# Optimization experiments

Hardware: AMD Instinct MI355X
Metric: run time of the kernel (lower is better)

## Reference

```python
import jax, jax.numpy as jnp
import numpy as np


def _graph_conv(feat, W, b, src, dst, num_nodes):
    """DGL GraphConv with norm='both', activation=relu.
    out = relu(D_in^{-1/2} * A * D_out^{-1/2} * (X @ W) + b)
    Degrees are clamped to a minimum of 1 (DGL behavior).
    """
    # Linear transform first (d_in == d_out here, order is math-equivalent)
    h = feat @ W  # [N, d_out]
    ones = jnp.ones(src.shape[0], dtype=feat.dtype)
    out_deg = jnp.clip(jax.ops.segment_sum(ones, src, num_segments=num_nodes), 1.0)
    in_deg = jnp.clip(jax.ops.segment_sum(ones, dst, num_segments=num_nodes), 1.0)
    norm_src = jax.lax.rsqrt(out_deg)  # [N]
    norm_dst = jax.lax.rsqrt(in_deg)   # [N]
    # gather messages from source nodes, scaled by src norm
    msg = h[src] * norm_src[src][:, None]  # [E, d_out]
    agg = jax.ops.segment_sum(msg, dst, num_segments=num_nodes)  # [N, d_out]
    return jax.nn.relu(agg * norm_dst[:, None] + b)


def setup_inputs() -> dict:
    key = jax.random.key(0)
    ks = jax.random.split(key, 8)
    N = 50000
    E_c, E_d = 1600000, 800000
    d_c, d_d = 128, 256
    feat_c = jax.random.normal(ks[0], (N, d_c), dtype=jnp.float32)
    feat_d = jax.random.normal(ks[1], (N, d_d), dtype=jnp.float32)
    src_c = jax.random.randint(ks[2], (E_c,), 0, N, dtype=jnp.int32)
    dst_c = jax.random.randint(ks[3], (E_c,), 0, N, dtype=jnp.int32)
    src_d = jax.random.randint(ks[4], (E_d,), 0, N, dtype=jnp.int32)
    dst_d = jax.random.randint(ks[5], (E_d,), 0, N, dtype=jnp.int32)
    W_c = jax.random.normal(ks[6], (d_c, d_c), dtype=jnp.float32) * (1.0 / np.sqrt(d_c))
    W_d = jax.random.normal(ks[7], (d_d, d_d), dtype=jnp.float32) * (1.0 / np.sqrt(d_d))
    b_c = jnp.zeros((d_c,), dtype=jnp.float32)
    b_d = jnp.zeros((d_d,), dtype=jnp.float32)
    return {"feat_c": feat_c, "feat_d": feat_d, "src_c": src_c, "dst_c": dst_c,
            "src_d": src_d, "dst_d": dst_d, "W_c": W_c, "b_c": b_c,
            "W_d": W_d, "b_d": b_d}


def reference(feat_c, feat_d, src_c, dst_c, src_d, dst_d, W_c, b_c, W_d, b_d):
    N_c = feat_c.shape[0]
    N_d = feat_d.shape[0]
    homo_feature_c = _graph_conv(feat_c, W_c, b_c, src_c, dst_c, N_c)
    homo_feature_d = _graph_conv(feat_d, W_d, b_d, src_d, dst_d, N_d)
    return (homo_feature_c, homo_feature_d)
```

## Files before the change

kernel.cpp:

```cpp
#include <hip/hip_runtime.h>
#include <hip/hip_bf16.h>


typedef __attribute__((ext_vector_type(8))) short short8;
typedef __attribute__((ext_vector_type(4))) float f32x4;

#define RND 4096
#define CAPMAX 8960

static __device__ __forceinline__ ushort f2b(float f) {
    __hip_bfloat16 h = __float2bfloat16(f);
    return *reinterpret_cast<ushort*>(&h);
}
static __device__ __forceinline__ float b2f(ushort u) {
    union { unsigned int i; float f; } c;
    c.i = ((unsigned int)u) << 16;
    return c.f;
}
static __device__ __forceinline__ void gld_lds16(const void* g, void* l) {
    __builtin_amdgcn_global_load_lds(
        (const __attribute__((address_space(1))) unsigned int*)g,
        (__attribute__((address_space(3))) unsigned int*)l, 16, 0, 0);
}

__global__ __launch_bounds__(256) void part_kernel(
    const int* __restrict__ src_c, const int* __restrict__ dst_c, int Ec, int Rc,
    const int* __restrict__ src_d, const int* __restrict__ dst_d, int Ed, int Rd,
    int* gf_cd, int* gf_cs, int* gf_dd, int* gf_ds,
    int* dbuf_c, int* sbuf_c, int* dbuf_d, int* sbuf_d, int capc, int capd)
{
    __shared__ int pk[RND];
    __shared__ unsigned char pb[RND];
    __shared__ int hist[256], st[256], ex2[256], cur[256], gbase[256];

    const int tid = threadIdx.x;
    const int bid = blockIdx.x;
    const int* keys; const int* pays; int E; int* gf; int* buf; int cap; int e0;
    if (bid < Rc)            { keys = dst_c; pays = src_c; E = Ec; gf = gf_cd; buf = dbuf_c; cap = capc; e0 = bid * RND; }
    else if (bid < 2 * Rc)   { keys = src_c; pays = 0;     E = Ec; gf = gf_cs; buf = sbuf_c; cap = capc; e0 = (bid - Rc) * RND; }
    else if (bid < 2 * Rc + Rd) { keys = dst_d; pays = src_d; E = Ed; gf = gf_dd; buf = dbuf_d; cap = capd; e0 = (bid - 2 * Rc) * RND; }
    else                     { keys = src_d; pays = 0;     E = Ed; gf = gf_ds; buf = sbuf_d; cap = capd; e0 = (bid - 2 * Rc - Rd) * RND; }

    hist[tid] = 0;
    __syncthreads();

    int kb[RND / 256], pv[RND / 256];
    int n = 0;
#pragma unroll
    for (int r = 0; r < RND / 256; ++r) {
        int e = e0 + r * 256 + tid;
        if (e < E) {
            int k = keys[e];
            pv[r] = pays ? ((pays[e] << 8) | (k & 255)) : k;
            kb[r] = k >> 8;
            atomicAdd(&hist[kb[r]], 1);
            n = r + 1;
        }
    }
    __syncthreads();

    int x = hist[tid];
    st[tid] = x;
    __syncthreads();
    for (int off = 1; off < 256; off <<= 1) {
        int t2 = 0;
        if (tid >= off) t2 = st[tid - off];
        __syncthreads();
        if (tid >= off) st[tid] += t2;
        __syncthreads();
    }
    ex2[tid] = st[tid] - x;
    cur[tid] = st[tid] - x;
    __syncthreads();

    for (int r = 0; r < n; ++r) {
        int slot = atomicAdd(&cur[kb[r]], 1);
        pk[slot] = pv[r];
        pb[slot] = (unsigned char)kb[r];
    }
    if (x) gbase[tid] = atomicAdd(&gf[tid], x);
    __syncthreads();

    int m = st[255];
    for (int i = tid; i < m; i += 256) {
        int b = pb[i];
        int pos = gbase[b] + (i - ex2[b]);
        if (pos < cap) buf[(size_t)b * cap + pos] = pk[i];
    }
}

__global__ __launch_bounds__(256) void b2s_kernel(
    const int* __restrict__ sbuf_c, const int* __restrict__ gf_cs, int capc, int* cnt_c,
    const int* __restrict__ sbuf_d, const int* __restrict__ gf_ds, int capd, int* cnt_d,
    int N, int NBKT)
{
    __shared__ int h[256];
    const int tid = threadIdx.x;
    const int* sbuf; const int* gf; int cap; int* cnt; int bb;
    if ((int)blockIdx.x < NBKT) { sbuf = sbuf_c; gf = gf_cs; cap = capc; cnt = cnt_c; bb = blockIdx.x; }
    else { sbuf = sbuf_d; gf = gf_ds; cap = capd; cnt = cnt_d; bb = blockIdx.x - NBKT; }
    h[tid] = 0;
    __syncthreads();
    int m = gf[bb]; if (m > cap) m = cap;
    const int* reg = sbuf + (size_t)bb * cap;
    for (int i = tid; i < m; i += 256) atomicAdd(&h[reg[i] & 255], 1);
    __syncthreads();
    int v = bb * 256 + tid;
    if (v < N) cnt[v] = h[tid];
}

__global__ __launch_bounds__(256) void b2d_kernel(
    int* dbuf_c, const int* __restrict__ gf_cd, int capc, int* rs_c, int* dg_c,
    int* dbuf_d, const int* __restrict__ gf_dd, int capd, int* rs_d, int* dg_d,
    int N, int NBKT)
{
    __shared__ int pk[CAPMAX];
    __shared__ int h[256], st[256], ex2[256], cur[256];
    const int tid = threadIdx.x;
    int* bbuf; const int* gf; int cap; int* rs; int* dg; int bb;
    if ((int)blockIdx.x < NBKT) { bbuf = dbuf_c; gf = gf_cd; cap = capc; rs = rs_c; dg = dg_c; bb = blockIdx.x; }
    else { bbuf = dbuf_d; gf = gf_dd; cap = capd; rs = rs_d; dg = dg_d; bb = blockIdx.x - NBKT; }

    int m = gf[bb]; if (m > cap) m = cap;
    int* reg = bbuf + (size_t)bb * cap;

    h[tid] = 0;
    __syncthreads();
    for (int i = tid; i < m; i += 256) atomicAdd(&h[reg[i] & 255], 1);
    __syncthreads();
    int x = h[tid];
    st[tid] = x;
    __syncthreads();
    for (int off = 1; off < 256; off <<= 1) {
        int t2 = 0;
        if (tid >= off) t2 = st[tid - off];
        __syncthreads();
        if (tid >= off) st[tid] += t2;
        __syncthreads();
    }
    int ex_t = st[tid] - x;
    ex2[tid] = ex_t;
    cur[tid] = ex_t;
    int v = bb * 256 + tid;
    if (v < N) { rs[v] = bb * cap + ex_t; dg[v] = x; }
    __syncthreads();
    for (int i = tid; i < m; i += 256) {
        int p = reg[i];
        int slot = atomicAdd(&cur[p & 255], 1);
        pk[slot] = p >> 8;
    }
    __syncthreads();
    for (int i = tid; i < m; i += 256) reg[i] = pk[i];
}

__global__ __launch_bounds__(256) void wprep_kernel(
    const float* __restrict__ Wc, const float* __restrict__ Wd,
    ushort* __restrict__ Wtc, ushort* __restrict__ Wtd)
{
    int t = blockIdx.x * 256 + threadIdx.x;
    ushort o[8];
    if (t < 2048) {
        int n = t >> 4, slot = t & 15;
        int k0 = (slot ^ (n & 7)) << 3;
#pragma unroll
        for (int j = 0; j < 8; ++j) o[j] = f2b(Wc[(k0 + j) * 128 + n]);
        uint4 vv;
        vv.x = (unsigned)o[0] | ((unsigned)o[1] << 16);
        vv.y = (unsigned)o[2] | ((unsigned)o[3] << 16);
        vv.z = (unsigned)o[4] | ((unsigned)o[5] << 16);
        vv.w = (unsigned)o[6] | ((unsigned)o[7] << 16);
        *(uint4*)&Wtc[n * 128 + slot * 8] = vv;
    } else if (t < 2048 + 8192) {
        int tt = t - 2048;
        int ci = tt >> 11, r = tt & 2047;
        int n = r >> 3, slot = r & 7;
        int k0 = ci * 64 + ((slot ^ (n & 7)) << 3);
#pragma unroll
        for (int j = 0; j < 8; ++j) o[j] = f2b(Wd[(k0 + j) * 256 + n]);
        uint4 vv;
        vv.x = (unsigned)o[0] | ((unsigned)o[1] << 16);
        vv.y = (unsigned)o[2] | ((unsigned)o[3] << 16);
        vv.z = (unsigned)o[4] | ((unsigned)o[5] << 16);
        vv.w = (unsigned)o[6] | ((unsigned)o[7] << 16);
        *(uint4*)&Wtd[ci * 16384 + n * 64 + slot * 8] = vv;
    }
}

__global__ __launch_bounds__(256) void cast_kernel(
    const float* __restrict__ Xc, const int* __restrict__ coc, ushort* __restrict__ Xbc,
    const float* __restrict__ Xd, const int* __restrict__ cod, ushort* __restrict__ Xbd,
    int N, int nbc)
{
    const float* X; const int* co; ushort* Xb; int C4, t;
    if ((int)blockIdx.x < nbc) { X = Xc; co = coc; Xb = Xbc; C4 = 32; t = blockIdx.x * 256 + threadIdx.x; }
    else { X = Xd; co = cod; Xb = Xbd; C4 = 64; t = (blockIdx.x - nbc) * 256 + threadIdx.x; }
    if (t >= N * C4) return;
    int row = t / C4, c4 = t % C4;
    int od = co[row]; if (od < 1) od = 1;
    float nr = rsqrtf((float)od);
    float4 xv = ((const float4*)(X + (size_t)row * (C4 * 4)))[c4];
    ushort4 o;
    o.x = f2b(xv.x * nr); o.y = f2b(xv.y * nr);
    o.z = f2b(xv.z * nr); o.w = f2b(xv.w * nr);
    ((ushort4*)(Xb + (size_t)row * (C4 * 4)))[c4] = o;
}

template <int VEC>
static __device__ __forceinline__ void agg_node(
    const ushort* __restrict__ Xb, const int* __restrict__ rs,
    const int* __restrict__ dg, const int* __restrict__ csr,
    float* __restrict__ out, int w, int lane, int N)
{
    constexpr int D = VEC * 64;
    if (w >= N) return;
    int beg = rs[w], deg = dg[w];
    float acc[VEC];
#pragma unroll
    for (int k = 0; k < VEC; ++k) acc[k] = 0.f;
    const int* rowp = csr + beg;

    for (int base = 0; base < deg; base += 64) {
        int m = deg - base; if (m > 64) m = 64;
        int u_l = (lane < m) ? rowp[base + lane] : 0;
#pragma unroll 4
        for (int j = 0; j < m; ++j) {
            int u = __shfl(u_l, j);
            const ushort* xr = Xb + (size_t)u * D + lane * VEC;
            if constexpr (VEC == 2) {
                unsigned int xv = *(const unsigned int*)xr;
                acc[0] += b2f((ushort)(xv & 0xffff));
                acc[1] += b2f((ushort)(xv >> 16));
            } else {
                uint2 xv = *(const uint2*)xr;
                acc[0] += b2f((ushort)(xv.x & 0xffff));
                acc[1] += b2f((ushort)(xv.x >> 16));
                acc[2] += b2f((ushort)(xv.y & 0xffff));
                acc[3] += b2f((ushort)(xv.y >> 16));
            }
        }
    }
    int id = deg < 1 ? 1 : deg;
    float nd = rsqrtf((float)id);
    float* orow = out + (size_t)w * D + lane * VEC;
    if constexpr (VEC == 2) {
        float2 o; o.x = acc[0] * nd; o.y = acc[1] * nd;
        *(float2*)orow = o;
    } else {
        float4 o; o.x = acc[0] * nd; o.y = acc[1] * nd;
        o.z = acc[2] * nd; o.w = acc[3] * nd;
        *(float4*)orow = o;
    }
}

__global__ __launch_bounds__(256) void agg_kernel2(
    const ushort* __restrict__ Xbc, const int* __restrict__ rsc,
    const int* __restrict__ dgc, const int* __restrict__ csrc, float* outc,
    const ushort* __restrict__ Xbd, const int* __restrict__ rsd,
    const int* __restrict__ dgd, const int* __restrict__ csrd, float* outd,
    int N, int abc)
{
    int lane = threadIdx.x & 63;
    if ((int)blockIdx.x < abc) {
        int w = (blockIdx.x * 256 + threadIdx.x) >> 6;
        agg_node<2>(Xbc, rsc, dgc, csrc, outc, w, lane, N);
    } else {
        int w = ((blockIdx.x - abc) * 256 + threadIdx.x) >> 6;
        agg_node<4>(Xbd, rsd, dgd, csrd, outd, w, lane, N);
    }
}

template <int K, int BN, int BK>
__global__ __launch_bounds__(256) void gemm2_kernel(
    const float* A, const ushort* __restrict__ Wt,
    const float* __restrict__ bias, float* O, int M)
{
    constexpr int BM = 64;
    constexpr int HN = BN / 2;
    constexpr int NC = HN / 16;
    constexpr int C4 = K / 4;
    __shared__ ushort Als[BM * K];
    __shared__ ushort Wts[BN * BK];

    const int tid = threadIdx.x;
    const int lane = tid & 63, wid = tid >> 6;
    const int wr = wid >> 1, wc = wid & 1;
    const int lr = lane & 15, lk8 = (lane >> 4) * 8;
    const int row0 = blockIdx.x * BM;

    f32x4 acc[2][NC];
#pragma unroll
    for (int mr = 0; mr < 2; ++mr)
#pragma unroll
        for (int nc = 0; nc < NC; ++nc) acc[mr][nc] = (f32x4)0.f;

    for (int i = tid; i < BM * C4; i += 256) {
        int r = i / C4, c4 = i % C4;
        int row = row0 + r;
        float4 x = make_float4(0.f, 0.f, 0.f, 0.f);
        if (row < M) x = *(const float4*)(A + (size_t)row * K + c4 * 4);
        ushort4 o;
        o.x = f2b(x.x); o.y = f2b(x.y); o.z = f2b(x.z); o.w = f2b(x.w);
        int slot = (c4 >> 1) ^ (r & 7);
        *(ushort4*)&Als[r * K + slot * 8 + (c4 & 1) * 4] = o;
    }

    for (int ci = 0; ci < K / BK; ++ci) {
        if (ci) __syncthreads();
        constexpr int NL = BN * BK * 2 / (256 * 16);
        const ushort* wsrc = Wt + ci * (BN * BK);
#pragma unroll
        for (int it = 0; it < NL; ++it) {
            int off16 = it * 256 + tid;
            gld_lds16(&wsrc[off16 * 8], &Wts[off16 * 8]);
        }
        __syncthreads();

#pragma unroll
        for (int k0 = 0; k0 < BK; k0 += 32) {
            short8 a[2], bfr[NC];
#pragma unroll
            for (int mr = 0; mr < 2; ++mr) {
                int r = wr * 32 + mr * 16 + lr;
                int k = ci * BK + k0 + lk8;
                int slot = (k >> 3) ^ (r & 7);
                a[mr] = *(const short8*)&Als[r * K + slot * 8];
            }
#pragma unroll
            for (int nc = 0; nc < NC; ++nc) {
                int n = wc * HN + nc * 16 + lr;
                int kk = k0 + lk8;
                int slot = (kk >> 3) ^ (n & 7);
                bfr[nc] = *(const short8*)&Wts[n * BK + slot * 8];
            }
#pragma unroll
            for (int mr = 0; mr < 2; ++mr)
#pragma unroll
                for (int nc = 0; nc < NC; ++nc)
                    acc[mr][nc] = __builtin_amdgcn_mfma_f32_16x16x32_bf16(
                        a[mr], bfr[nc], acc[mr][nc], 0, 0, 0);
        }
    }

#pragma unroll
    for (int mr = 0; mr < 2; ++mr)
#pragma unroll
        for (int nc = 0; nc < NC; ++nc) {
            int col = wc * HN + nc * 16 + lr;
            float bv = bias[col];
#pragma unroll
            for (int r = 0; r < 4; ++r) {
                int row = row0 + wr * 32 + mr * 16 + (lane >> 4) * 4 + r;
                if (row < M)
                    O[(size_t)row * BN + col] = fmaxf(acc[mr][nc][r] + bv, 0.f);
            }
        }
}

extern "C" void kernel_launch(void* const* d_in, const int* in_sizes, int n_in,
                              void* d_out, int out_size, void* d_ws, size_t ws_size,
                              hipStream_t stream)
{
    const float* feat_c = (const float*)d_in[0];
    const float* feat_d = (const float*)d_in[1];
    const int* src_c = (const int*)d_in[2];
    const int* dst_c = (const int*)d_in[3];
    const int* src_d = (const int*)d_in[4];
    const int* dst_d = (const int*)d_in[5];
    const float* W_c = (const float*)d_in[6];
    const float* b_c = (const float*)d_in[7];
    const float* W_d = (const float*)d_in[8];
    const float* b_d = (const float*)d_in[9];

    const int D_c = in_sizes[7];
    const int D_d = in_sizes[9];
    const int N = in_sizes[0] / D_c;
    const int E_c = in_sizes[2];
    const int E_d = in_sizes[4];

    float* out_c = (float*)d_out;
    float* out_d = (float*)d_out + (size_t)N * D_c;

    const int NBKT = (N + 255) >> 8;
    int capc = E_c / NBKT; capc += 8 * (int)sqrtf((float)capc) + 32; capc = (capc + 15) & ~15;
    int capd = E_d / NBKT; capd += 8 * (int)sqrtf((float)capd) + 32; capd = (capd + 15) & ~15;
    if (capc > CAPMAX) capc = CAPMAX;
    if (capd > CAPMAX) capd = CAPMAX;

    int* ws = (int*)d_ws;
    int* cnt_out_c = ws;
    int* cnt_out_d = ws + N;
    int* gf_cd = ws + 2 * (size_t)N;
    int* gf_cs = gf_cd + 256;
    int* gf_dd = gf_cs + 256;
    int* gf_ds = gf_dd + 256;
    int* rs_c  = gf_ds + 256;
    int* dg_c  = rs_c + N;
    int* rs_d  = dg_c + N;
    int* dg_d  = rs_d + N;
    ushort* Wt_c = (ushort*)(dg_d + N);
    ushort* Wt_d = Wt_c + 16384;
    int* dbuf_c = (int*)(Wt_d + 65536);
    int* sbuf_c = dbuf_c + (size_t)NBKT * capc;
    int* dbuf_d = sbuf_c + (size_t)NBKT * capc;
    int* sbuf_d = dbuf_d + (size_t)NBKT * capd;
    ushort* Xb_c = (ushort*)(sbuf_d + (size_t)NBKT * capd);
    ushort* Xb_d = Xb_c + (size_t)N * D_c;

    hipMemsetAsync(gf_cd, 0, 1024 * sizeof(int), stream);

    wprep_kernel<<<40, 256, 0, stream>>>(W_c, W_d, Wt_c, Wt_d);

    const int Rc = (E_c + RND - 1) / RND;
    const int Rd = (E_d + RND - 1) / RND;
    part_kernel<<<2 * (Rc + Rd), 256, 0, stream>>>(
        src_c, dst_c, E_c, Rc, src_d, dst_d, E_d, Rd,
        gf_cd, gf_cs, gf_dd, gf_ds,
        dbuf_c, sbuf_c, dbuf_d, sbuf_d, capc, capd);

    b2s_kernel<<<2 * NBKT, 256, 0, stream>>>(
        sbuf_c, gf_cs, capc, cnt_out_c,
        sbuf_d, gf_ds, capd, cnt_out_d, N, NBKT);

    int nbc = (N * (D_c / 4) + 255) / 256, nbd = (N * (D_d / 4) + 255) / 256;
    cast_kernel<<<nbc + nbd, 256, 0, stream>>>(feat_c, cnt_out_c, Xb_c,
                                               feat_d, cnt_out_d, Xb_d, N, nbc);

    b2d_kernel<<<2 * NBKT, 256, 0, stream>>>(
        dbuf_c, gf_cd, capc, rs_c, dg_c,
        dbuf_d, gf_dd, capd, rs_d, dg_d, N, NBKT);

    int abc = (N + 3) / 4;
    agg_kernel2<<<2 * abc, 256, 0, stream>>>(Xb_c, rs_c, dg_c, dbuf_c, out_c,
                                             Xb_d, rs_d, dg_d, dbuf_d, out_d, N, abc);

    int gb = (N + 63) / 64;
    gemm2_kernel<128, 128, 128><<<gb, 256, 0, stream>>>(out_c, Wt_c, b_c, out_c, N);
    gemm2_kernel<256, 256, 64><<<gb, 256, 0, stream>>>(out_d, Wt_d, b_d, out_d, N);
}
```

Before: 418.0 us.

## Fuse neighbor aggregation with the bf16 MFMA GEMM epilogue into one kernel

Replaces the separate aggregation kernel and the two GEMM kernels with one kernel. Each 512-thread block aggregates 32 destination nodes into a bf16 LDS tile, then multiplies that tile by W using MFMA and applies bias and ReLU. This removes the fp32 round trip of the aggregated features through global memory and two kernel launches. In exchange, every block reloads W into LDS for only 32 rows, uses more LDS per block (which can lower occupancy), and runs GEMM waves that each handle only 16 rows.

```diff
diff --git a/kernel.cpp b/kernel.cpp
--- a/kernel.cpp
+++ b/kernel.cpp
@@ -206,154 +206,137 @@
 }
 
 template <int VEC>
-static __device__ __forceinline__ void agg_node(
-    const ushort* __restrict__ Xb, const int* __restrict__ rs,
+static __device__ __forceinline__ void fused_branch(
+    int blk, const ushort* __restrict__ Xb, const int* __restrict__ rs,
     const int* __restrict__ dg, const int* __restrict__ csr,
-    float* __restrict__ out, int w, int lane, int N)
+    const ushort* __restrict__ Wt, const float* __restrict__ bias,
+    float* __restrict__ out, int N, ushort* At, ushort* Wls)
 {
     constexpr int D = VEC * 64;
-    if (w >= N) return;
-    int beg = rs[w], deg = dg[w];
-    float acc[VEC];
-#pragma unroll
-    for (int k = 0; k < VEC; ++k) acc[k] = 0.f;
-    const int* rowp = csr + beg;
-
-    for (int base = 0; base < deg; base += 64) {
-        int m = deg - base; if (m > 64) m = 64;
-        int u_l = (lane < m) ? rowp[base + lane] : 0;
-#pragma unroll 4
-        for (int j = 0; j < m; ++j) {
-            int u = __shfl(u_l, j);
-            const ushort* xr = Xb + (size_t)u * D + lane * VEC;
-            if constexpr (VEC == 2) {
-                unsigned int xv = *(const unsigned int*)xr;
-                acc[0] += b2f((ushort)(xv & 0xffff));
-                acc[1] += b2f((ushort)(xv >> 16));
-            } else {
-                uint2 xv = *(const uint2*)xr;
-                acc[0] += b2f((ushort)(xv.x & 0xffff));
-                acc[1] += b2f((ushort)(xv.x >> 16));
-                acc[2] += b2f((ushort)(xv.y & 0xffff));
-                acc[3] += b2f((ushort)(xv.y >> 16));
-            }
-        }
-    }
-    int id = deg < 1 ? 1 : deg;
-    float nd = rsqrtf((float)id);
-    float* orow = out + (size_t)w * D + lane * VEC;
-    if constexpr (VEC == 2) {
-        float2 o; o.x = acc[0] * nd; o.y = acc[1] * nd;
-        *(float2*)orow = o;
-    } else {
-        float4 o; o.x = acc[0] * nd; o.y = acc[1] * nd;
-        o.z = acc[2] * nd; o.w = acc[3] * nd;
-        *(float4*)orow = o;
-    }
-}
-
-__global__ __launch_bounds__(256) void agg_kernel2(
-    const ushort* __restrict__ Xbc, const int* __restrict__ rsc,
-    const int* __restrict__ dgc, const int* __restrict__ csrc, float* outc,
-    const ushort* __restrict__ Xbd, const int* __restrict__ rsd,
-    const int* __restrict__ dgd, const int* __restrict__ csrd, float* outd,
-    int N, int abc)
-{
-    int lane = threadIdx.x & 63;
-    if ((int)blockIdx.x < abc) {
-        int w = (blockIdx.x * 256 + threadIdx.x) >> 6;
-        agg_node<2>(Xbc, rsc, dgc, csrc, outc, w, lane, N);
-    } else {
-        int w = ((blockIdx.x - abc) * 256 + threadIdx.x) >> 6;
-        agg_node<4>(Xbd, rsd, dgd, csrd, outd, w, lane, N);
-    }
-}
-
-template <int K, int BN, int BK>
-__global__ __launch_bounds__(256) void gemm2_kernel(
-    const float* A, const ushort* __restrict__ Wt,
-    const float* __restrict__ bias, float* O, int M)
-{
-    constexpr int BM = 64;
-    constexpr int HN = BN / 2;
-    constexpr int NC = HN / 16;
-    constexpr int C4 = K / 4;
-    __shared__ ushort Als[BM * K];
-    __shared__ ushort Wts[BN * BK];
-
+    constexpr int NCH = (D * D) / 16384;
+    constexpr int BK = D / NCH;
+    constexpr int NC = D / 64;
     const int tid = threadIdx.x;
     const int lane = tid & 63, wid = tid >> 6;
-    const int wr = wid >> 1, wc = wid & 1;
+
+#pragma unroll
+    for (int it = 0; it < 4; ++it) {
+        int off16 = it * 512 + tid;
+        gld_lds16(&Wt[off16 * 8], &Wls[off16 * 8]);
+    }
+
+    const int node0 = blk * 32;
+#pragma unroll
+    for (int s = 0; s < 4; ++s) {
+        const int row = wid * 4 + s;
+        const int v = node0 + row;
+        float acc[VEC];
+#pragma unroll
+        for (int k = 0; k < VEC; ++k) acc[k] = 0.f;
+        int deg = 0;
+        if (v < N) {
+            deg = dg[v];
+            const int* rowp = csr + rs[v];
+            for (int base = 0; base < deg; base += 64) {
+                int m = deg - base; if (m > 64) m = 64;
+                int u_l = (lane < m) ? rowp[base + lane] : 0;
+#pragma unroll 8
+                for (int j = 0; j < m; ++j) {
+                    int u = __shfl(u_l, j);
+                    const ushort* xr = Xb + (size_t)u * D + lane * VEC;
+                    if constexpr (VEC == 2) {
+                        unsigned int xv = *(const unsigned int*)xr;
+                        acc[0] += b2f((ushort)(xv & 0xffff));
+                        acc[1] += b2f((ushort)(xv >> 16));
+                    } else {
+                        uint2 xv = *(const uint2*)xr;
+                        acc[0] += b2f((ushort)(xv.x & 0xffff));
+                        acc[1] += b2f((ushort)(xv.x >> 16));
+                        acc[2] += b2f((ushort)(xv.y & 0xffff));
+                        acc[3] += b2f((ushort)(xv.y >> 16));
+                    }
+                }
+            }
+        }
+        float nd = rsqrtf((float)(deg < 1 ? 1 : deg));
+        const int k0 = lane * VEC;
+        const int slot = (k0 >> 3) ^ (row & 7);
+        ushort* dstp = &At[row * D + slot * 8 + (k0 & 7)];
+        if constexpr (VEC == 2) {
+            unsigned int pk = (unsigned)f2b(acc[0] * nd) | ((unsigned)f2b(acc[1] * nd) << 16);
+            *(unsigned int*)dstp = pk;
+        } else {
+            uint2 pk;
+            pk.x = (unsigned)f2b(acc[0] * nd) | ((unsigned)f2b(acc[1] * nd) << 16);
+            pk.y = (unsigned)f2b(acc[2] * nd) | ((unsigned)f2b(acc[3] * nd) << 16);
+            *(uint2*)dstp = pk;
+        }
+    }
+    __syncthreads();
+
+    const int wr = wid >> 2, wc = wid & 3;
     const int lr = lane & 15, lk8 = (lane >> 4) * 8;
-    const int row0 = blockIdx.x * BM;
-
-    f32x4 acc[2][NC];
-#pragma unroll
-    for (int mr = 0; mr < 2; ++mr)
-#pragma unroll
-        for (int nc = 0; nc < NC; ++nc) acc[mr][nc] = (f32x4)0.f;
-
-    for (int i = tid; i < BM * C4; i += 256) {
-        int r = i / C4, c4 = i % C4;
-        int row = row0 + r;
-        float4 x = make_float4(0.f, 0.f, 0.f, 0.f);
-        if (row < M) x = *(const float4*)(A + (size_t)row * K + c4 * 4);
-        ushort4 o;
-        o.x = f2b(x.x); o.y = f2b(x.y); o.z = f2b(x.z); o.w = f2b(x.w);
-        int slot = (c4 >> 1) ^ (r & 7);
-        *(ushort4*)&Als[r * K + slot * 8 + (c4 & 1) * 4] = o;
-    }
-
-    for (int ci = 0; ci < K / BK; ++ci) {
-        if (ci) __syncthreads();
-        constexpr int NL = BN * BK * 2 / (256 * 16);
-        const ushort* wsrc = Wt + ci * (BN * BK);
-#pragma unroll
-        for (int it = 0; it < NL; ++it) {
-            int off16 = it * 256 + tid;
-            gld_lds16(&wsrc[off16 * 8], &Wts[off16 * 8]);
-        }
-        __syncthreads();
-
+    f32x4 acc[NC];
+#pragma unroll
+    for (int nc = 0; nc < NC; ++nc) acc[nc] = (f32x4)0.f;
+
+#pragma unroll
+    for (int ci = 0; ci < NCH; ++ci) {
+        if (ci) {
+            __syncthreads();
+#pragma unroll
+            for (int it = 0; it < 4; ++it) {
+                int off16 = it * 512 + tid;
+                gld_lds16(&Wt[ci * 16384 + off16 * 8], &Wls[off16 * 8]);
+            }
+            __syncthreads();
+        }
 #pragma unroll
         for (int k0 = 0; k0 < BK; k0 += 32) {
-            short8 a[2], bfr[NC];
-#pragma unroll
-            for (int mr = 0; mr < 2; ++mr) {
-                int r = wr * 32 + mr * 16 + lr;
-                int k = ci * BK + k0 + lk8;
-                int slot = (k >> 3) ^ (r & 7);
-                a[mr] = *(const short8*)&Als[r * K + slot * 8];
+            const int r = wr * 16 + lr;
+            const int kg = ci * BK + k0 + lk8;
+            const int aslot = (kg >> 3) ^ (r & 7);
+            short8 a = *(const short8*)&At[r * D + aslot * 8];
+#pragma unroll
+            for (int nc = 0; nc < NC; ++nc) {
+                const int n = wc * (NC * 16) + nc * 16 + lr;
+                const int kk = k0 + lk8;
+                const int bslot = (kk >> 3) ^ (n & 7);
+                short8 b = *(const short8*)&Wls[n * BK + bslot * 8];
+                acc[nc] = __builtin_amdgcn_mfma_f32_16x16x32_bf16(a, b, acc[nc], 0, 0, 0);
             }
-#pragma unroll
-            for (int nc = 0; nc < NC; ++nc) {
-                int n = wc * HN + nc * 16 + lr;
-                int kk = k0 + lk8;
-                int slot = (kk >> 3) ^ (n & 7);
-                bfr[nc] = *(const short8*)&Wts[n * BK + slot * 8];
-            }
-#pragma unroll
-            for (int mr = 0; mr < 2; ++mr)
-#pragma unroll
-                for (int nc = 0; nc < NC; ++nc)
-                    acc[mr][nc] = __builtin_amdgcn_mfma_f32_16x16x32_bf16(
-                        a[mr], bfr[nc], acc[mr][nc], 0, 0, 0);
-        }
-    }
-
-#pragma unroll
-    for (int mr = 0; mr < 2; ++mr)
-#pragma unroll
-        for (int nc = 0; nc < NC; ++nc) {
-            int col = wc * HN + nc * 16 + lr;
-            float bv = bias[col];
-#pragma unroll
-            for (int r = 0; r < 4; ++r) {
-                int row = row0 + wr * 32 + mr * 16 + (lane >> 4) * 4 + r;
-                if (row < M)
-                    O[(size_t)row * BN + col] = fmaxf(acc[mr][nc][r] + bv, 0.f);
-            }
-        }
+        }
+    }
+
+#pragma unroll
+    for (int nc = 0; nc < NC; ++nc) {
+        const int col = wc * (NC * 16) + nc * 16 + lr;
+        const float bv = bias[col];
+#pragma unroll
+        for (int r4 = 0; r4 < 4; ++r4) {
+            const int row = wr * 16 + (lane >> 4) * 4 + r4;
+            const int v = node0 + row;
+            if (v < N)
+                out[(size_t)v * D + col] = fmaxf(acc[nc][r4] + bv, 0.f);
+        }
+    }
+}
+
+__global__ __launch_bounds__(512) void fused_kernel(
+    const ushort* __restrict__ Xbc, const int* __restrict__ rsc,
+    const int* __restrict__ dgc, const int* __restrict__ csrc,
+    const ushort* __restrict__ Wtc, const float* __restrict__ bc, float* outc,
+    const ushort* __restrict__ Xbd, const int* __restrict__ rsd,
+    const int* __restrict__ dgd, const int* __restrict__ csrd,
+    const ushort* __restrict__ Wtd, const float* __restrict__ bd, float* outd,
+    int N, int nblkc)
+{
+    __shared__ ushort At[32 * 256];
+    __shared__ ushort Wls[16384];
+    if ((int)blockIdx.x < nblkc)
+        fused_branch<2>(blockIdx.x, Xbc, rsc, dgc, csrc, Wtc, bc, outc, N, At, Wls);
+    else
+        fused_branch<4>(blockIdx.x - nblkc, Xbd, rsd, dgd, csrd, Wtd, bd, outd, N, At, Wls);
 }
 
 extern "C" void kernel_launch(void* const* d_in, const int* in_sizes, int n_in,
@@ -429,11 +412,8 @@
         dbuf_c, gf_cd, capc, rs_c, dg_c,
         dbuf_d, gf_dd, capd, rs_d, dg_d, N, NBKT);
 
-    int abc = (N + 3) / 4;
-    agg_kernel2<<<2 * abc, 256, 0, stream>>>(Xb_c, rs_c, dg_c, dbuf_c, out_c,
-                                             Xb_d, rs_d, dg_d, dbuf_d, out_d, N, abc);
-
-    int gb = (N + 63) / 64;
-    gemm2_kernel<128, 128, 128><<<gb, 256, 0, stream>>>(out_c, Wt_c, b_c, out_c, N);
-    gemm2_kernel<256, 256, 64><<<gb, 256, 0, stream>>>(out_d, Wt_d, b_d, out_d, N);
-}
+    const int nblk = (N + 31) / 32;
+    fused_kernel<<<2 * nblk, 512, 0, stream>>>(
+        Xb_c, rs_c, dg_c, dbuf_c, Wt_c, b_c, out_c,
+        Xb_d, rs_d, dg_d, dbuf_d, Wt_d, b_d, out_d, N, nblk);
+}
```

After: 442.9 us. 1.06x slower.
